# Optimization experiments

Measured on AMD Instinct MI355X. Metric: run time of the kernel, lower is better.

Reference implementation:

```python
import jax, jax.numpy as jnp
import numpy as np

N = 100000   # nodes
E = 800000   # edges (before self-loops)
IN = 256     # in_channels
HID = 32     # hidden_channels per head
H = 8        # heads in layer 1
OUT = 40     # num classes
NEG_SLOPE = 0.2  # PyG GATConv default


def gat_conv(x, src, dst, W, att_src, att_dst, bias, concat):
    """PyG-style GATConv (inference). x:[N,F], W:[F,H*C], att_*:[H,C], bias:[H*C or C]."""
    n = x.shape[0]
    heads, ch = att_src.shape
    h = (x @ W).reshape(n, heads, ch)                      # [N,H,C]
    a_src = (h * att_src[None]).sum(-1)                    # [N,H]
    a_dst = (h * att_dst[None]).sum(-1)                    # [N,H]
    logits = a_src[src] + a_dst[dst]                       # [E,H]
    logits = jax.nn.leaky_relu(logits, NEG_SLOPE)
    # segment softmax over destination nodes
    m = jax.ops.segment_max(logits, dst, num_segments=n)   # [N,H]
    m = jnp.where(jnp.isfinite(m), m, 0.0)                 # guard empty segments
    ex = jnp.exp(logits - m[dst])                          # [E,H]
    denom = jax.ops.segment_sum(ex, dst, num_segments=n)   # [N,H]
    alpha = ex / (denom[dst] + 1e-16)                      # [E,H]
    msg = h[src] * alpha[..., None]                        # [E,H,C]
    out = jax.ops.segment_sum(msg, dst, num_segments=n)    # [N,H,C]
    out = out.reshape(n, heads * ch) if concat else out.mean(axis=1)
    return out + bias


def setup_inputs() -> dict:
    key = jax.random.key(0)
    ks = jax.random.split(key, 10)
    x = jax.random.normal(ks[0], (N, IN), jnp.float32)
    edge_index = jax.random.randint(ks[1], (2, E), 0, N, dtype=jnp.int32)
    W1 = jax.random.normal(ks[2], (IN, H * HID), jnp.float32) / np.sqrt(IN)
    att_src1 = jax.random.normal(ks[3], (H, HID), jnp.float32) / np.sqrt(HID)
    att_dst1 = jax.random.normal(ks[4], (H, HID), jnp.float32) / np.sqrt(HID)
    b1 = jnp.zeros((H * HID,), jnp.float32)
    W2 = jax.random.normal(ks[5], (H * HID, OUT), jnp.float32) / np.sqrt(H * HID)
    att_src2 = jax.random.normal(ks[6], (1, OUT), jnp.float32) / np.sqrt(OUT)
    att_dst2 = jax.random.normal(ks[7], (1, OUT), jnp.float32) / np.sqrt(OUT)
    b2 = jnp.zeros((OUT,), jnp.float32)
    return {"x": x, "edge_index": edge_index, "W1": W1, "att_src1": att_src1,
            "att_dst1": att_dst1, "b1": b1, "W2": W2, "att_src2": att_src2,
            "att_dst2": att_dst2, "b2": b2}


def reference(x, edge_index, W1, att_src1, att_dst1, b1, W2, att_src2, att_dst2, b2):
    # add self-loops (PyG GATConv default)
    loops = jnp.arange(N, dtype=edge_index.dtype)
    src = jnp.concatenate([edge_index[0], loops])
    dst = jnp.concatenate([edge_index[1], loops])
    h = gat_conv(x, src, dst, W1, att_src1, att_dst1, b1, concat=True)
    h = jax.nn.elu(h)
    return gat_conv(h, src, dst, W2, att_src2, att_dst2, b2, concat=False)
```

## Files before the change

### kernel.cpp

```cpp
#include <hip/hip_runtime.h>
#include <math.h>

#define NSLOPE 0.2f

__device__ __forceinline__ float lrelu(float x){ return x > 0.f ? x : NSLOPE * x; }
__device__ __forceinline__ float eluf(float x){ return x > 0.f ? x : expm1f(x); }

__device__ __forceinline__ unsigned short f2bf(float f) {
  unsigned u = __float_as_uint(f);
  u = (u + 0x7fff + ((u >> 16) & 1)) >> 16;
  return (unsigned short)u;
}
__device__ __forceinline__ unsigned pk2bf(float a, float b) {
  return (unsigned)f2bf(a) | ((unsigned)f2bf(b) << 16);
}

typedef __attribute__((ext_vector_type(8))) short bf16x8;
typedef __attribute__((ext_vector_type(4))) float f32x4;

__global__ __launch_bounds__(256) void conv_w_kernel(const float* __restrict__ W,
                                                     unsigned short* __restrict__ wt) {
  int n = blockIdx.x;
  int k = threadIdx.x;
  wt[n * 256 + k] = f2bf(W[k * 256 + n]);
}

__global__ __launch_bounds__(256) void gemm1_mfma_kernel(const float* __restrict__ x,
                                                         const unsigned short* __restrict__ wt,
                                                         unsigned short* __restrict__ h1b,
                                                         int N) {
  __shared__ __align__(16) unsigned short Asl[128][40];
  __shared__ __align__(16) unsigned short Bsl[128][40];
  int tid = threadIdx.x;
  int bm = blockIdx.x >> 1, bn = blockIdx.x & 1;
  int row0 = bm * 128, col0 = bn * 128;

  int lr = tid >> 2;
  int lk = (tid & 3) * 8;

  int lane = tid & 63, wv = tid >> 6;
  int m0 = (wv & 1) * 64, n0 = (wv >> 1) * 64;
  int lm = lane & 15, quad = lane >> 4;

  f32x4 acc[4][4];
#pragma unroll
  for (int i = 0; i < 4; ++i)
#pragma unroll
    for (int j = 0; j < 4; ++j) acc[i][j] = (f32x4){0.f, 0.f, 0.f, 0.f};

  for (int kc = 0; kc < 256; kc += 32) {
    float4 a0 = {0,0,0,0}, a1 = {0,0,0,0}, a2 = {0,0,0,0}, a3 = {0,0,0,0};
    int r0 = row0 + lr, r1 = row0 + 64 + lr;
    if (r0 < N) {
      const float4* s0 = (const float4*)(x + (size_t)r0 * 256 + kc + lk);
      a0 = s0[0]; a1 = s0[1];
    }
    if (r1 < N) {
      const float4* s1 = (const float4*)(x + (size_t)r1 * 256 + kc + lk);
      a2 = s1[0]; a3 = s1[1];
    }
    uint4 bv0 = *(const uint4*)(wt + (size_t)(col0 + lr) * 256 + kc + lk);
    uint4 bv1 = *(const uint4*)(wt + (size_t)(col0 + 64 + lr) * 256 + kc + lk);
    uint4 pa0, pa1;
    pa0.x = pk2bf(a0.x, a0.y); pa0.y = pk2bf(a0.z, a0.w);
    pa0.z = pk2bf(a1.x, a1.y); pa0.w = pk2bf(a1.z, a1.w);
    pa1.x = pk2bf(a2.x, a2.y); pa1.y = pk2bf(a2.z, a2.w);
    pa1.z = pk2bf(a3.x, a3.y); pa1.w = pk2bf(a3.z, a3.w);
    __syncthreads();
    *(uint4*)&Asl[lr][lk]      = pa0;
    *(uint4*)&Asl[64 + lr][lk] = pa1;
    *(uint4*)&Bsl[lr][lk]      = bv0;
    *(uint4*)&Bsl[64 + lr][lk] = bv1;
    __syncthreads();
    bf16x8 aF[4], bF[4];
#pragma unroll
    for (int i = 0; i < 4; ++i) aF[i] = *(const bf16x8*)&Asl[m0 + i * 16 + lm][quad * 8];
#pragma unroll
    for (int j = 0; j < 4; ++j) bF[j] = *(const bf16x8*)&Bsl[n0 + j * 16 + lm][quad * 8];
#pragma unroll
    for (int i = 0; i < 4; ++i)
#pragma unroll
      for (int j = 0; j < 4; ++j)
        acc[i][j] = __builtin_amdgcn_mfma_f32_16x16x32_bf16(aF[i], bF[j], acc[i][j], 0, 0, 0);
  }

#pragma unroll
  for (int i = 0; i < 4; ++i) {
#pragma unroll
    for (int j = 0; j < 4; ++j) {
      int gc = col0 + n0 + j * 16 + lm;
      int grb = row0 + m0 + i * 16 + quad * 4;
#pragma unroll
      for (int r = 0; r < 4; ++r) {
        int grow = grb + r;
        if (grow < N) h1b[(size_t)grow * 256 + gc] = f2bf(acc[i][j][r]);
      }
    }
  }
}

__global__ __launch_bounds__(256) void att1_kernel(const unsigned short* __restrict__ h1b,
                                                   const float* __restrict__ att_src,
                                                   const float* __restrict__ att_dst,
                                                   float* __restrict__ a_src,
                                                   float* __restrict__ a_dst, int N) {
  __shared__ float sas[256];
  __shared__ float sad[256];
  int tid = threadIdx.x;
  sas[tid] = att_src[tid];
  sad[tid] = att_dst[tid];
  __syncthreads();
  int gid = blockIdx.x * 256 + tid;
  if (gid >= N * 8) return;
  int h = gid & 7;
  const uint4* hv = (const uint4*)(h1b + (size_t)(gid >> 3) * 256 + h * 32);
  float s1 = 0.f, s2 = 0.f;
#pragma unroll
  for (int q = 0; q < 4; ++q) {
    uint4 u = hv[q];
    unsigned uu[4] = {u.x, u.y, u.z, u.w};
#pragma unroll
    for (int e = 0; e < 4; ++e) {
      float lo = __uint_as_float(uu[e] << 16);
      float hi = __uint_as_float(uu[e] & 0xffff0000u);
      int c = h * 32 + q * 8 + e * 2;
      s1 += lo * sas[c] + hi * sas[c + 1];
      s2 += lo * sad[c] + hi * sad[c + 1];
    }
  }
  a_src[gid] = s1;
  a_dst[gid] = s2;
}

__global__ void count_kernel(const int* __restrict__ ei, int* __restrict__ cnt, int E, int N) {
  int e = blockIdx.x * 256 + threadIdx.x;
  if (e >= E + N) return;
  int d = (e < E) ? ei[E + e] : (e - E);
  atomicAdd(&cnt[d], 1);
}

__global__ __launch_bounds__(256) void scan1_kernel(const int* __restrict__ cnt,
                                                    int* __restrict__ tmp,
                                                    int* __restrict__ bsum, int N) {
  __shared__ int sh[256];
  int t = threadIdx.x;
  int base = blockIdx.x * 1024 + t * 4;
  int v[4]; int s = 0;
#pragma unroll
  for (int j = 0; j < 4; ++j) { v[j] = (base + j < N) ? cnt[base + j] : 0; s += v[j]; }
  sh[t] = s;
  __syncthreads();
  for (int off = 1; off < 256; off <<= 1) {
    int xv = (t >= off) ? sh[t - off] : 0;
    __syncthreads();
    sh[t] += xv;
    __syncthreads();
  }
  if (t == 255) bsum[blockIdx.x] = sh[255];
  int run = sh[t] - s;
#pragma unroll
  for (int j = 0; j < 4; ++j) {
    if (base + j < N) tmp[base + j] = run;
    run += v[j];
  }
}

__global__ __launch_bounds__(128) void scan2_kernel(const int* __restrict__ bsum,
                                                    int* __restrict__ boff, int nb) {
  __shared__ int sh[128];
  int t = threadIdx.x;
  int v = (t < nb) ? bsum[t] : 0;
  sh[t] = v;
  __syncthreads();
  for (int off = 1; off < 128; off <<= 1) {
    int xv = (t >= off) ? sh[t - off] : 0;
    __syncthreads();
    sh[t] += xv;
    __syncthreads();
  }
  if (t < nb) boff[t] = sh[t] - v;
}

__global__ void scan3_kernel(const int* __restrict__ tmp, const int* __restrict__ boff,
                             int* __restrict__ row_ptr, int* __restrict__ cursor,
                             int N, int Etot) {
  int i = blockIdx.x * 256 + threadIdx.x;
  if (i == 0) row_ptr[N] = Etot;
  if (i >= N) return;
  int rp = tmp[i] + boff[i >> 10];
  row_ptr[i] = rp;
  cursor[i] = rp;
}

__global__ void fill_kernel(const int* __restrict__ ei, int* __restrict__ cursor,
                            int* __restrict__ col, int E, int N) {
  int e = blockIdx.x * 256 + threadIdx.x;
  if (e >= E + N) return;
  int s, d;
  if (e < E) { s = ei[e]; d = ei[E + e]; } else { s = e - E; d = s; }
  int pos = atomicAdd(&cursor[d], 1);
  col[pos] = s;
}

__global__ __launch_bounds__(256) void agg1_kernel(const unsigned short* __restrict__ h1b,
                                                   const float* __restrict__ a_src,
                                                   const float* __restrict__ a_dst,
                                                   const int* __restrict__ row_ptr,
                                                   const int* __restrict__ col,
                                                   const float* __restrict__ b1,
                                                   unsigned short* __restrict__ hmidb, int N) {
  int lane = threadIdx.x & 63;
  int n = blockIdx.x * 4 + (threadIdx.x >> 6);
  if (n >= N) return;
  int beg = row_ptr[n], deg = row_ptr[n + 1] - beg;

  int hA = lane & 7, eoA = lane >> 3;
  float adst = a_dst[n * 8 + hA];
  float den = 0.f;
  for (int e0 = 0; e0 < deg; e0 += 8) {
    int e = e0 + eoA;
    if (e < deg) den += __expf(lrelu(a_src[col[beg + e] * 8 + hA] + adst));
  }
#pragma unroll
  for (int off = 8; off < 64; off <<= 1) den += __shfl_xor(den, off);
  float invden = 1.f / (den + 1e-16f);

  int half = lane >> 5;
  int cl = lane & 31;
  int hB = cl >> 2;
  float4 acc0 = {0.f,0.f,0.f,0.f}, acc1 = {0.f,0.f,0.f,0.f};

  for (int c0 = 0; c0 < deg; c0 += 8) {
    int eb = c0 + eoA;
    int ec = eb < deg ? eb : deg - 1;
    int sB = col[beg + ec];
    float alB = 0.f;
    if (eb < deg) alB = __expf(lrelu(a_src[sB * 8 + hA] + adst)) * invden;
    int rem = deg - c0; if (rem > 8) rem = 8;
#pragma unroll
    for (int p = 0; p < 4; ++p) {
      int myE = 2 * p + half;
      int s = __shfl(sB, myE * 8);
      float al = __shfl(alB, myE * 8 + hB);
      if (myE < rem) {
        uint4 hv = *(const uint4*)(h1b + (size_t)s * 256 + cl * 8);
        acc0.x = fmaf(al, __uint_as_float(hv.x << 16), acc0.x);
        acc0.y = fmaf(al, __uint_as_float(hv.x & 0xffff0000u), acc0.y);
        acc0.z = fmaf(al, __uint_as_float(hv.y << 16), acc0.z);
        acc0.w = fmaf(al, __uint_as_float(hv.y & 0xffff0000u), acc0.w);
        acc1.x = fmaf(al, __uint_as_float(hv.z << 16), acc1.x);
        acc1.y = fmaf(al, __uint_as_float(hv.z & 0xffff0000u), acc1.y);
        acc1.z = fmaf(al, __uint_as_float(hv.w << 16), acc1.z);
        acc1.w = fmaf(al, __uint_as_float(hv.w & 0xffff0000u), acc1.w);
      }
    }
  }
  float po[8] = {acc0.x, acc0.y, acc0.z, acc0.w, acc1.x, acc1.y, acc1.z, acc1.w};
#pragma unroll
  for (int j = 0; j < 8; ++j) po[j] += __shfl(po[j], cl + 32);
  if (half == 0) {
    const float4* b4 = (const float4*)(b1 + cl * 8);
    float4 bb0 = b4[0], bb1 = b4[1];
    float r0 = eluf(po[0] + bb0.x), r1 = eluf(po[1] + bb0.y);
    float r2 = eluf(po[2] + bb0.z), r3 = eluf(po[3] + bb0.w);
    float r4 = eluf(po[4] + bb1.x), r5 = eluf(po[5] + bb1.y);
    float r6 = eluf(po[6] + bb1.z), r7 = eluf(po[7] + bb1.w);
    uint4 ov;
    ov.x = pk2bf(r0, r1); ov.y = pk2bf(r2, r3);
    ov.z = pk2bf(r4, r5); ov.w = pk2bf(r6, r7);
    *(uint4*)(hmidb + (size_t)n * 256 + cl * 8) = ov;
  }
}

__global__ __launch_bounds__(256) void gemm2_mfma_kernel(const unsigned short* __restrict__ hmidb,
                                                         const float* __restrict__ W2,
                                                         const float* __restrict__ as2,
                                                         const float* __restrict__ ad2,
                                                         unsigned short* __restrict__ h2b,
                                                         float* __restrict__ a_src2,
                                                         float* __restrict__ a_dst2, int N) {
  __shared__ __align__(16) unsigned short Asl[128][40];
  __shared__ __align__(16) unsigned short Bs[48][264];
  __shared__ float asv[48], adv[48];
  int tid = threadIdx.x;
  for (int i = tid; i < 48 * 264 / 2; i += 256) ((unsigned*)Bs)[i] = 0;
  if (tid < 48) {
    asv[tid] = (tid < 40) ? as2[tid] : 0.f;
    adv[tid] = (tid < 40) ? ad2[tid] : 0.f;
  }
  __syncthreads();
  for (int i = tid; i < 256 * 40; i += 256) {
    int k = i / 40, c = i - k * 40;
    Bs[c][k] = f2bf(W2[i]);
  }

  int row0 = blockIdx.x * 128;
  int lane = tid & 63, wv = tid >> 6;
  int lm = lane & 15, quad = lane >> 4;
  int lr = tid >> 1;
  int lk = (tid & 1) * 16;

  f32x4 acc[2][3];
#pragma unroll
  for (int i = 0; i < 2; ++i)
#pragma unroll
    for (int j = 0; j < 3; ++j) acc[i][j] = (f32x4){0.f,0.f,0.f,0.f};

  for (int kc = 0; kc < 256; kc += 32) {
    uint4 v0 = {0,0,0,0}, v1 = {0,0,0,0};
    int r = row0 + lr;
    if (r < N) {
      const uint4* src = (const uint4*)(hmidb + (size_t)r * 256 + kc + lk);
      v0 = src[0]; v1 = src[1];
    }
    __syncthreads();
    *(uint4*)&Asl[lr][lk]     = v0;
    *(uint4*)&Asl[lr][lk + 8] = v1;
    __syncthreads();
    bf16x8 aF[2], bF[3];
#pragma unroll
    for (int i = 0; i < 2; ++i) aF[i] = *(const bf16x8*)&Asl[wv * 32 + i * 16 + lm][quad * 8];
#pragma unroll
    for (int j = 0; j < 3; ++j) bF[j] = *(const bf16x8*)&Bs[j * 16 + lm][kc + quad * 8];
#pragma unroll
    for (int i = 0; i < 2; ++i)
#pragma unroll
      for (int j = 0; j < 3; ++j)
        acc[i][j] = __builtin_amdgcn_mfma_f32_16x16x32_bf16(aF[i], bF[j], acc[i][j], 0, 0, 0);
  }

#pragma unroll
  for (int i = 0; i < 2; ++i) {
#pragma unroll
    for (int r = 0; r < 4; ++r) {
      int grow = row0 + wv * 32 + i * 16 + quad * 4 + r;
      float vs = 0.f, vd = 0.f;
#pragma unroll
      for (int j = 0; j < 3; ++j) {
        vs = fmaf(acc[i][j][r], asv[j * 16 + lm], vs);
        vd = fmaf(acc[i][j][r], adv[j * 16 + lm], vd);
      }
#pragma unroll
      for (int off = 1; off < 16; off <<= 1) {
        vs += __shfl_xor(vs, off);
        vd += __shfl_xor(vd, off);
      }
      if (grow < N) {
#pragma unroll
        for (int j = 0; j < 3; ++j) {
          int c = j * 16 + lm;
          if (c < 40) h2b[(size_t)grow * 40 + c] = f2bf(acc[i][j][r]);
        }
        if (lm == 0) { a_src2[grow] = vs; a_dst2[grow] = vd; }
      }
    }
  }
}

__global__ __launch_bounds__(256) void agg2_kernel(const unsigned short* __restrict__ h2b,
                                                   const float* __restrict__ a_src,
                                                   const float* __restrict__ a_dst,
                                                   const int* __restrict__ row_ptr,
                                                   const int* __restrict__ col,
                                                   const float* __restrict__ b2,
                                                   float* __restrict__ out, int N) {
  int lane = threadIdx.x & 63;
  int n = blockIdx.x * 4 + (threadIdx.x >> 6);
  if (n >= N) return;
  int beg = row_ptr[n], deg = row_ptr[n + 1] - beg;
  float adst = a_dst[n];
  float den = 0.f;
  for (int e0 = 0; e0 < deg; e0 += 64) {
    int e = e0 + lane;
    if (e < deg) den += __expf(lrelu(a_src[col[beg + e]] + adst));
  }
#pragma unroll
  for (int off = 1; off < 64; off <<= 1) den += __shfl_xor(den, off);
  float invden = 1.f / (den + 1e-16f);

  int eg = lane / 10;
  int cg = lane % 10;
  bool active = lane < 60;
  float4 acc = {0.f,0.f,0.f,0.f};
  for (int c0 = 0; c0 < deg; c0 += 6) {
    int e = c0 + eg;
    bool on = active && (e < deg);
    int ec = e < deg ? e : deg - 1;
    int s = col[beg + ec];
    if (on) {
      float al = __expf(lrelu(a_src[s] + adst)) * invden;
      uint2 hv = *(const uint2*)(h2b + (size_t)s * 40 + cg * 4);
      acc.x = fmaf(al, __uint_as_float(hv.x << 16), acc.x);
      acc.y = fmaf(al, __uint_as_float(hv.x & 0xffff0000u), acc.y);
      acc.z = fmaf(al, __uint_as_float(hv.y << 16), acc.z);
      acc.w = fmaf(al, __uint_as_float(hv.y & 0xffff0000u), acc.w);
    }
  }
  float4 o = acc;
#pragma unroll
  for (int k = 1; k < 6; ++k) {
    int src = lane + 10 * k;
    o.x += __shfl(acc.x, src);
    o.y += __shfl(acc.y, src);
    o.z += __shfl(acc.z, src);
    o.w += __shfl(acc.w, src);
  }
  if (lane < 10) {
    float4 bb = *(const float4*)(b2 + cg * 4);
    o.x += bb.x; o.y += bb.y; o.z += bb.z; o.w += bb.w;
    *(float4*)(out + (size_t)n * 40 + cg * 4) = o;
  }
}

extern "C" void kernel_launch(void* const* d_in, const int* in_sizes, int n_in,
                              void* d_out, int out_size, void* d_ws, size_t ws_size,
                              hipStream_t stream) {
  const float* x   = (const float*)d_in[0];
  const int*   ei  = (const int*)d_in[1];
  const float* W1  = (const float*)d_in[2];
  const float* as1 = (const float*)d_in[3];
  const float* ad1 = (const float*)d_in[4];
  const float* b1  = (const float*)d_in[5];
  const float* W2  = (const float*)d_in[6];
  const float* as2 = (const float*)d_in[7];
  const float* ad2 = (const float*)d_in[8];
  const float* b2  = (const float*)d_in[9];
  float* out = (float*)d_out;

  int N = in_sizes[0] / 256;
  int E = in_sizes[1] / 2;
  int Etot = E + N;

  char* p = (char*)d_ws;
  auto alloc = [&](size_t bytes) -> char* {
    char* r = p;
    p += (bytes + 255) & ~(size_t)255;
    return r;
  };
  unsigned short* w1t   = (unsigned short*)alloc((size_t)256 * 256 * 2);
  unsigned short* h1b   = (unsigned short*)alloc((size_t)N * 256 * 2);
  unsigned short* hmidb = (unsigned short*)alloc((size_t)N * 256 * 2);
  unsigned short* h2b   = (unsigned short*)alloc((size_t)N * 40 * 2);
  float* a_src1 = (float*)alloc((size_t)N * 8 * 4);
  float* a_dst1 = (float*)alloc((size_t)N * 8 * 4);
  float* a_src2 = (float*)alloc((size_t)N * 4);
  float* a_dst2 = (float*)alloc((size_t)N * 4);
  int* cnt      = (int*)alloc((size_t)N * 4);
  int* cursor   = (int*)alloc((size_t)N * 4);
  int* row_ptr  = (int*)alloc(((size_t)N + 1) * 4);
  int* tmp      = (int*)alloc((size_t)N * 4);
  int* bsum     = (int*)alloc(512);
  int* boff     = (int*)alloc(512);
  int* colx     = (int*)alloc((size_t)Etot * 4);

  hipMemsetAsync(cnt, 0, (size_t)N * 4, stream);

  int nbE = (Etot + 255) / 256;
  int nb1 = (N + 1023) / 1024;
  count_kernel<<<nbE, 256, 0, stream>>>(ei, cnt, E, N);
  scan1_kernel<<<nb1, 256, 0, stream>>>(cnt, tmp, bsum, N);
  scan2_kernel<<<1, 128, 0, stream>>>(bsum, boff, nb1);
  scan3_kernel<<<(N + 255) / 256, 256, 0, stream>>>(tmp, boff, row_ptr, cursor, N, Etot);
  fill_kernel<<<nbE, 256, 0, stream>>>(ei, cursor, colx, E, N);

  conv_w_kernel<<<256, 256, 0, stream>>>(W1, w1t);
  gemm1_mfma_kernel<<<((N + 127) / 128) * 2, 256, 0, stream>>>(x, w1t, h1b, N);
  att1_kernel<<<(N * 8 + 255) / 256, 256, 0, stream>>>(h1b, as1, ad1, a_src1, a_dst1, N);
  agg1_kernel<<<(N + 3) / 4, 256, 0, stream>>>(h1b, a_src1, a_dst1, row_ptr, colx, b1, hmidb, N);
  gemm2_mfma_kernel<<<(N + 127) / 128, 256, 0, stream>>>(hmidb, W2, as2, ad2, h2b, a_src2, a_dst2, N);
  agg2_kernel<<<(N + 3) / 4, 256, 0, stream>>>(h2b, a_src2, a_dst2, row_ptr, colx, b2, out, N);
}
```

Measured before the change: 465.3 us.

## Fuse softmax denominator into aggregation pass and collapse scan into single kernel

Both aggregation kernels now accumulate unnormalized exp-weighted messages and the softmax denominator in one pass over neighbours, normalizing at the end. This removes the separate gather of col and a_src for the denominator. In agg2, edge indices and exp values are computed once per 60-edge chunk and broadcast by shuffle rather than recomputed per lane group. The three-kernel prefix scan is replaced by one single-block 1024-thread scan with serial per-thread chunks, cutting launches at the cost of low parallelism and strided, uncoalesced cnt reads.

```diff
diff --git a/kernel.cpp b/kernel.cpp
--- a/kernel.cpp
+++ b/kernel.cpp
@@ -139,57 +139,33 @@
   atomicAdd(&cnt[d], 1);
 }
 
-__global__ __launch_bounds__(256) void scan1_kernel(const int* __restrict__ cnt,
-                                                    int* __restrict__ tmp,
-                                                    int* __restrict__ bsum, int N) {
-  __shared__ int sh[256];
+__global__ __launch_bounds__(1024) void scan_kernel(const int* __restrict__ cnt,
+                                                    int* __restrict__ row_ptr,
+                                                    int* __restrict__ cursor,
+                                                    int N, int Etot) {
+  __shared__ int sh[1024];
   int t = threadIdx.x;
-  int base = blockIdx.x * 1024 + t * 4;
-  int v[4]; int s = 0;
-#pragma unroll
-  for (int j = 0; j < 4; ++j) { v[j] = (base + j < N) ? cnt[base + j] : 0; s += v[j]; }
+  int per = (N + 1023) / 1024;
+  int lo = t * per, hi = lo + per;
+  if (hi > N) hi = N;
+  int s = 0;
+  for (int i = lo; i < hi; ++i) s += cnt[i];
   sh[t] = s;
   __syncthreads();
-  for (int off = 1; off < 256; off <<= 1) {
-    int xv = (t >= off) ? sh[t - off] : 0;
-    __syncthreads();
-    sh[t] += xv;
-    __syncthreads();
-  }
-  if (t == 255) bsum[blockIdx.x] = sh[255];
+  for (int off = 1; off < 1024; off <<= 1) {
+    int v = (t >= off) ? sh[t - off] : 0;
+    __syncthreads();
+    sh[t] += v;
+    __syncthreads();
+  }
   int run = sh[t] - s;
-#pragma unroll
-  for (int j = 0; j < 4; ++j) {
-    if (base + j < N) tmp[base + j] = run;
-    run += v[j];
-  }
-}
-
-__global__ __launch_bounds__(128) void scan2_kernel(const int* __restrict__ bsum,
-                                                    int* __restrict__ boff, int nb) {
-  __shared__ int sh[128];
-  int t = threadIdx.x;
-  int v = (t < nb) ? bsum[t] : 0;
-  sh[t] = v;
-  __syncthreads();
-  for (int off = 1; off < 128; off <<= 1) {
-    int xv = (t >= off) ? sh[t - off] : 0;
-    __syncthreads();
-    sh[t] += xv;
-    __syncthreads();
-  }
-  if (t < nb) boff[t] = sh[t] - v;
-}
-
-__global__ void scan3_kernel(const int* __restrict__ tmp, const int* __restrict__ boff,
-                             int* __restrict__ row_ptr, int* __restrict__ cursor,
-                             int N, int Etot) {
-  int i = blockIdx.x * 256 + threadIdx.x;
-  if (i == 0) row_ptr[N] = Etot;
-  if (i >= N) return;
-  int rp = tmp[i] + boff[i >> 10];
-  row_ptr[i] = rp;
-  cursor[i] = rp;
+  for (int i = lo; i < hi; ++i) {
+    int c = cnt[i];
+    row_ptr[i] = run;
+    cursor[i] = run;
+    run += c;
+  }
+  if (t == 1023) row_ptr[N] = Etot;
 }
 
 __global__ void fill_kernel(const int* __restrict__ ei, int* __restrict__ cursor,
@@ -216,32 +192,26 @@
 
   int hA = lane & 7, eoA = lane >> 3;
   float adst = a_dst[n * 8 + hA];
-  float den = 0.f;
-  for (int e0 = 0; e0 < deg; e0 += 8) {
-    int e = e0 + eoA;
-    if (e < deg) den += __expf(lrelu(a_src[col[beg + e] * 8 + hA] + adst));
-  }
-#pragma unroll
-  for (int off = 8; off < 64; off <<= 1) den += __shfl_xor(den, off);
-  float invden = 1.f / (den + 1e-16f);
 
   int half = lane >> 5;
   int cl = lane & 31;
   int hB = cl >> 2;
   float4 acc0 = {0.f,0.f,0.f,0.f}, acc1 = {0.f,0.f,0.f,0.f};
+  float den = 0.f;
 
   for (int c0 = 0; c0 < deg; c0 += 8) {
     int eb = c0 + eoA;
     int ec = eb < deg ? eb : deg - 1;
     int sB = col[beg + ec];
-    float alB = 0.f;
-    if (eb < deg) alB = __expf(lrelu(a_src[sB * 8 + hA] + adst)) * invden;
+    float exB = 0.f;
+    if (eb < deg) exB = __expf(lrelu(a_src[sB * 8 + hA] + adst));
+    den += exB;
     int rem = deg - c0; if (rem > 8) rem = 8;
 #pragma unroll
     for (int p = 0; p < 4; ++p) {
       int myE = 2 * p + half;
       int s = __shfl(sB, myE * 8);
-      float al = __shfl(alB, myE * 8 + hB);
+      float al = __shfl(exB, myE * 8 + hB);
       if (myE < rem) {
         uint4 hv = *(const uint4*)(h1b + (size_t)s * 256 + cl * 8);
         acc0.x = fmaf(al, __uint_as_float(hv.x << 16), acc0.x);
@@ -255,16 +225,21 @@
       }
     }
   }
+#pragma unroll
+  for (int off = 8; off < 64; off <<= 1) den += __shfl_xor(den, off);
+  float invden = 1.f / (den + 1e-16f);
+  float invB = __shfl(invden, hB);
+
   float po[8] = {acc0.x, acc0.y, acc0.z, acc0.w, acc1.x, acc1.y, acc1.z, acc1.w};
 #pragma unroll
   for (int j = 0; j < 8; ++j) po[j] += __shfl(po[j], cl + 32);
   if (half == 0) {
     const float4* b4 = (const float4*)(b1 + cl * 8);
     float4 bb0 = b4[0], bb1 = b4[1];
-    float r0 = eluf(po[0] + bb0.x), r1 = eluf(po[1] + bb0.y);
-    float r2 = eluf(po[2] + bb0.z), r3 = eluf(po[3] + bb0.w);
-    float r4 = eluf(po[4] + bb1.x), r5 = eluf(po[5] + bb1.y);
-    float r6 = eluf(po[6] + bb1.z), r7 = eluf(po[7] + bb1.w);
+    float r0 = eluf(fmaf(po[0], invB, bb0.x)), r1 = eluf(fmaf(po[1], invB, bb0.y));
+    float r2 = eluf(fmaf(po[2], invB, bb0.z)), r3 = eluf(fmaf(po[3], invB, bb0.w));
+    float r4 = eluf(fmaf(po[4], invB, bb1.x)), r5 = eluf(fmaf(po[5], invB, bb1.y));
+    float r6 = eluf(fmaf(po[6], invB, bb1.z)), r7 = eluf(fmaf(po[7], invB, bb1.w));
     uint4 ov;
     ov.x = pk2bf(r0, r1); ov.y = pk2bf(r2, r3);
     ov.z = pk2bf(r4, r5); ov.w = pk2bf(r6, r7);
@@ -369,33 +344,39 @@
   if (n >= N) return;
   int beg = row_ptr[n], deg = row_ptr[n + 1] - beg;
   float adst = a_dst[n];
-  float den = 0.f;
-  for (int e0 = 0; e0 < deg; e0 += 64) {
-    int e = e0 + lane;
-    if (e < deg) den += __expf(lrelu(a_src[col[beg + e]] + adst));
-  }
-#pragma unroll
-  for (int off = 1; off < 64; off <<= 1) den += __shfl_xor(den, off);
-  float invden = 1.f / (den + 1e-16f);
 
   int eg = lane / 10;
   int cg = lane % 10;
   bool active = lane < 60;
   float4 acc = {0.f,0.f,0.f,0.f};
-  for (int c0 = 0; c0 < deg; c0 += 6) {
-    int e = c0 + eg;
-    bool on = active && (e < deg);
-    int ec = e < deg ? e : deg - 1;
-    int s = col[beg + ec];
-    if (on) {
-      float al = __expf(lrelu(a_src[s] + adst)) * invden;
-      uint2 hv = *(const uint2*)(h2b + (size_t)s * 40 + cg * 4);
-      acc.x = fmaf(al, __uint_as_float(hv.x << 16), acc.x);
-      acc.y = fmaf(al, __uint_as_float(hv.x & 0xffff0000u), acc.y);
-      acc.z = fmaf(al, __uint_as_float(hv.y << 16), acc.z);
-      acc.w = fmaf(al, __uint_as_float(hv.y & 0xffff0000u), acc.w);
-    }
-  }
+  float den = 0.f;
+
+  for (int c0 = 0; c0 < deg; c0 += 60) {
+    int eb = c0 + lane;
+    int ec = eb < deg ? eb : deg - 1;
+    int sB = col[beg + ec];
+    float ex = 0.f;
+    if (lane < 60 && eb < deg) ex = __expf(lrelu(a_src[sB] + adst));
+    den += ex;
+    int rem = deg - c0; if (rem > 60) rem = 60;
+    int nst = (rem + 5) / 6;
+    for (int st = 0; st < nst; ++st) {
+      int lsrc = st * 6 + eg;
+      float al = __shfl(ex, lsrc);
+      int s = __shfl(sB, lsrc);
+      if (active && (c0 + lsrc) < deg) {
+        uint2 hv = *(const uint2*)(h2b + (size_t)s * 40 + cg * 4);
+        acc.x = fmaf(al, __uint_as_float(hv.x << 16), acc.x);
+        acc.y = fmaf(al, __uint_as_float(hv.x & 0xffff0000u), acc.y);
+        acc.z = fmaf(al, __uint_as_float(hv.y << 16), acc.z);
+        acc.w = fmaf(al, __uint_as_float(hv.y & 0xffff0000u), acc.w);
+      }
+    }
+  }
+#pragma unroll
+  for (int off = 1; off < 64; off <<= 1) den += __shfl_xor(den, off);
+  float inv = 1.f / (den + 1e-16f);
+
   float4 o = acc;
 #pragma unroll
   for (int k = 1; k < 6; ++k) {
@@ -407,7 +388,10 @@
   }
   if (lane < 10) {
     float4 bb = *(const float4*)(b2 + cg * 4);
-    o.x += bb.x; o.y += bb.y; o.z += bb.z; o.w += bb.w;
+    o.x = fmaf(o.x, inv, bb.x);
+    o.y = fmaf(o.y, inv, bb.y);
+    o.z = fmaf(o.z, inv, bb.z);
+    o.w = fmaf(o.w, inv, bb.w);
     *(float4*)(out + (size_t)n * 40 + cg * 4) = o;
   }
 }
@@ -448,19 +432,13 @@
   int* cnt      = (int*)alloc((size_t)N * 4);
   int* cursor   = (int*)alloc((size_t)N * 4);
   int* row_ptr  = (int*)alloc(((size_t)N + 1) * 4);
-  int* tmp      = (int*)alloc((size_t)N * 4);
-  int* bsum     = (int*)alloc(512);
-  int* boff     = (int*)alloc(512);
   int* colx     = (int*)alloc((size_t)Etot * 4);
 
   hipMemsetAsync(cnt, 0, (size_t)N * 4, stream);
 
   int nbE = (Etot + 255) / 256;
-  int nb1 = (N + 1023) / 1024;
   count_kernel<<<nbE, 256, 0, stream>>>(ei, cnt, E, N);
-  scan1_kernel<<<nb1, 256, 0, stream>>>(cnt, tmp, bsum, N);
-  scan2_kernel<<<1, 128, 0, stream>>>(bsum, boff, nb1);
-  scan3_kernel<<<(N + 255) / 256, 256, 0, stream>>>(tmp, boff, row_ptr, cursor, N, Etot);
+  scan_kernel<<<1, 1024, 0, stream>>>(cnt, row_ptr, cursor, N, Etot);
   fill_kernel<<<nbE, 256, 0, stream>>>(ei, cursor, colx, E, N);
 
   conv_w_kernel<<<256, 256, 0, stream>>>(W1, w1t);
```

Measured after the change: 669.6 us. +43.9%, slower.
